# Optimization experiments

Hardware: AMD Instinct MI355X
Metric: run time of the kernel (lower is better)

The kernel has to match this reference:

```python
import jax, jax.numpy as jnp
import numpy as np

B, T, D, FF, H, K = 8, 1024, 512, 2048, 8, 15
HD = D // H  # key_dim = d_model // num_heads


def _ln(x, g, b):
    # keras LayerNormalization default epsilon = 1e-3
    m = jnp.mean(x, axis=-1, keepdims=True)
    v = jnp.var(x, axis=-1, keepdims=True)
    return (x - m) * jax.lax.rsqrt(v + 1e-3) * g + b


def setup_inputs() -> dict:
    key = jax.random.key(0)
    ks = iter(jax.random.split(key, 64))

    def rn(shape, s=0.02):
        return jax.random.normal(next(ks), shape, jnp.float32) * s

    p = {}
    p['x'] = jax.random.normal(next(ks), (B, T, D), jnp.float32)
    # ff_pre: LN -> Dense(FF, relu) -> Dense(D)
    p['g1'] = jnp.ones((D,), jnp.float32); p['b1'] = jnp.zeros((D,), jnp.float32)
    p['Wff1'] = rn((D, FF)); p['bff1'] = jnp.zeros((FF,), jnp.float32)
    p['Wff2'] = rn((FF, D)); p['bff2'] = jnp.zeros((D,), jnp.float32)
    # attention norm + MHA projections (keras EinsumDense shapes)
    p['ga'] = jnp.ones((D,), jnp.float32); p['ba'] = jnp.zeros((D,), jnp.float32)
    p['Wq'] = rn((D, H, HD)); p['bq'] = jnp.zeros((H, HD), jnp.float32)
    p['Wk'] = rn((D, H, HD)); p['bk'] = jnp.zeros((H, HD), jnp.float32)
    p['Wv'] = rn((D, H, HD)); p['bv'] = jnp.zeros((H, HD), jnp.float32)
    p['Wo'] = rn((H, HD, D)); p['bo'] = jnp.zeros((D,), jnp.float32)
    # conv branch: LN -> pointwise conv (2D, gelu) -> depthwise conv(k=15) -> BN -> swish -> pointwise conv (D)
    p['gc'] = jnp.ones((D,), jnp.float32); p['bc'] = jnp.zeros((D,), jnp.float32)
    p['Wcp'] = rn((D, 2 * D)); p['bcp'] = jnp.zeros((2 * D,), jnp.float32)
    p['dwk'] = rn((K, 1, 2 * D)); p['dwb'] = jnp.zeros((2 * D,), jnp.float32)
    p['bn_g'] = jnp.ones((2 * D,), jnp.float32); p['bn_b'] = jnp.zeros((2 * D,), jnp.float32)
    p['bn_m'] = jnp.zeros((2 * D,), jnp.float32)
    p['bn_v'] = jnp.ones((2 * D,), jnp.float32)
    p['Wco'] = rn((2 * D, D)); p['bco'] = jnp.zeros((D,), jnp.float32)
    # ff_post
    p['g2'] = jnp.ones((D,), jnp.float32); p['b2'] = jnp.zeros((D,), jnp.float32)
    p['Wf1'] = rn((D, FF)); p['bf1'] = jnp.zeros((FF,), jnp.float32)
    p['Wf2'] = rn((FF, D)); p['bf2'] = jnp.zeros((D,), jnp.float32)
    return p


def reference(x, g1, b1, Wff1, bff1, Wff2, bff2, ga, ba, Wq, bq, Wk, bk, Wv, bv, Wo, bo, gc, bc, Wcp, bcp, dwk, dwb, bn_g, bn_b, bn_m, bn_v, Wco, bco, g2, b2, Wf1, bf1, Wf2, bf2):
    # Macaron FFN (pre), half-step residual applied later
    x_ff = jnp.maximum(_ln(x, g1, b1) @ Wff1 + bff1, 0.0) @ Wff2 + bff2

    # causal multi-head self-attention (cache=None path)
    a = _ln(x, ga, ba)
    q = jnp.einsum('btd,dhk->bthk', a, Wq) + bq
    k = jnp.einsum('btd,dhk->bthk', a, Wk) + bk
    v = jnp.einsum('btd,dhk->bthk', a, Wv) + bv
    scores = jnp.einsum('bqhd,bkhd->bhqk', q, k) / jnp.sqrt(jnp.float32(HD))
    causal = jnp.tril(jnp.ones((T, T), bool))  # [T,T]
    scores = jnp.where(causal, scores, jnp.float32(-1e9))
    w = jax.nn.softmax(scores, axis=-1)
    ctx = jnp.einsum('bhqk,bkhd->bqhd', w, v)
    attn = jnp.einsum('bqhd,hdo->bqo', ctx, Wo) + bo

    x = x + 0.5 * x_ff + attn

    # convolution module: pointwise(gelu) -> causal left-pad -> depthwise -> BN(inference) -> swish -> pointwise
    c = jax.nn.gelu(_ln(x, gc, bc) @ Wcp + bcp, approximate=False)
    c = jnp.pad(c, ((0, 0), (K - 1, 0), (0, 0)))  # causal pad
    c = jax.lax.conv_general_dilated(
        c, dwk, window_strides=(1,), padding='VALID',
        dimension_numbers=('NWC', 'WIO', 'NWC'), feature_group_count=2 * D) + dwb
    c = (c - bn_m) * jax.lax.rsqrt(bn_v + 1e-3) * bn_g + bn_b
    c = c * jax.nn.sigmoid(c)  # swish
    c = c @ Wco + bco
    x = x + c

    # post FFN (full residual)
    x = x + (jnp.maximum(_ln(x, g2, b2) @ Wf1 + bf1, 0.0) @ Wf2 + bf2)
    return x
```

## Files before the change

kernel.cpp:

```cpp
#include <hip/hip_runtime.h>
#include <hip/hip_bf16.h>
#include <math.h>

#define BB 8
#define TT 1024
#define DD 512
#define FFD 2048
#define HH 8
#define HDD 64
#define KW 15
#define MR (BB*TT)
#define QKVN 1536

typedef __attribute__((ext_vector_type(8))) short short8;
typedef __attribute__((ext_vector_type(4))) short short4v;
typedef __attribute__((ext_vector_type(4))) float f32x4;
typedef __hip_bfloat16 bf16;

__device__ __forceinline__ float bf2f(unsigned u16) {
    return __uint_as_float(u16 << 16);
}

__device__ __forceinline__ void async_copy16(const void* g, void* l) {
    __builtin_amdgcn_global_load_lds(
        (const __attribute__((address_space(1))) void*)g,
        (__attribute__((address_space(3))) void*)l, 16, 0, 0);
}

__device__ __forceinline__ float gelu_exact(float v) {
    return 0.5f * v * (1.0f + erff(v * 0.70710678118654752f));
}

struct PrepPack {
    const float* src[10];
    bf16*        dst[10];
    int          K[10];
    int          lgNT[10];
    float        scale[10];
    int          off[10];
    const float* bq; const float* bk; const float* bv;
    float*       bdst;
    const float* x;
    const float* g1; const float* b1; const float* ga; const float* ba;
    bf16* o1; bf16* o2;
};

__global__ __launch_bounds__(256) void prep_kernel(PrepPack P) {
    __shared__ alignas(16) bf16 T[64][72];
    const int bid = blockIdx.x;
    if (bid == 1536) {
        #pragma unroll
        for (int it = 0; it < 6; ++it) {
            int i = it * 256 + threadIdx.x;
            float v = i < 512 ? P.bq[i] * 0.125f
                              : (i < 1024 ? P.bk[i - 512] : P.bv[i - 1024]);
            P.bdst[i] = v;
        }
        return;
    }
    if (bid > 1536) {
        int wave = ((bid - 1537) * 256 + (int)threadIdx.x) >> 6;
        int lane = threadIdx.x & 63;
        const float* row = P.x + (size_t)wave * DD;
        float4 v0 = ((const float4*)row)[lane];
        float4 v1 = ((const float4*)row)[64 + lane];
        float s  = v0.x + v0.y + v0.z + v0.w + v1.x + v1.y + v1.z + v1.w;
        float ss = v0.x*v0.x + v0.y*v0.y + v0.z*v0.z + v0.w*v0.w
                 + v1.x*v1.x + v1.y*v1.y + v1.z*v1.z + v1.w*v1.w;
        #pragma unroll
        for (int off = 32; off >= 1; off >>= 1) {
            s  += __shfl_xor(s,  off, 64);
            ss += __shfl_xor(ss, off, 64);
        }
        float mean = s * (1.0f / DD);
        float var  = ss * (1.0f / DD) - mean * mean;
        float r    = rsqrtf(var + 1e-3f);
        float n0x = (v0.x - mean) * r, n0y = (v0.y - mean) * r,
              n0z = (v0.z - mean) * r, n0w = (v0.w - mean) * r;
        float n1x = (v1.x - mean) * r, n1y = (v1.y - mean) * r,
              n1z = (v1.z - mean) * r, n1w = (v1.w - mean) * r;
        {
            float4 g0 = ((const float4*)P.g1)[lane];
            float4 gg = ((const float4*)P.g1)[64 + lane];
            float4 b0 = ((const float4*)P.b1)[lane];
            float4 bb = ((const float4*)P.b1)[64 + lane];
            alignas(8) bf16 o0[4], o1[4];
            o0[0] = __float2bfloat16(n0x * g0.x + b0.x);
            o0[1] = __float2bfloat16(n0y * g0.y + b0.y);
            o0[2] = __float2bfloat16(n0z * g0.z + b0.z);
            o0[3] = __float2bfloat16(n0w * g0.w + b0.w);
            o1[0] = __float2bfloat16(n1x * gg.x + bb.x);
            o1[1] = __float2bfloat16(n1y * gg.y + bb.y);
            o1[2] = __float2bfloat16(n1z * gg.z + bb.z);
            o1[3] = __float2bfloat16(n1w * gg.w + bb.w);
            bf16* orow = P.o1 + (size_t)wave * DD;
            *(short4v*)(orow + lane * 4)       = *(const short4v*)o0;
            *(short4v*)(orow + 256 + lane * 4) = *(const short4v*)o1;
        }
        {
            float4 g0 = ((const float4*)P.ga)[lane];
            float4 gg = ((const float4*)P.ga)[64 + lane];
            float4 b0 = ((const float4*)P.ba)[lane];
            float4 bb = ((const float4*)P.ba)[64 + lane];
            alignas(8) bf16 o0[4], o1[4];
            o0[0] = __float2bfloat16(n0x * g0.x + b0.x);
            o0[1] = __float2bfloat16(n0y * g0.y + b0.y);
            o0[2] = __float2bfloat16(n0z * g0.z + b0.z);
            o0[3] = __float2bfloat16(n0w * g0.w + b0.w);
            o1[0] = __float2bfloat16(n1x * gg.x + bb.x);
            o1[1] = __float2bfloat16(n1y * gg.y + bb.y);
            o1[2] = __float2bfloat16(n1z * gg.z + bb.z);
            o1[3] = __float2bfloat16(n1w * gg.w + bb.w);
            bf16* orow = P.o2 + (size_t)wave * DD;
            *(short4v*)(orow + lane * 4)       = *(const short4v*)o0;
            *(short4v*)(orow + 256 + lane * 4) = *(const short4v*)o1;
        }
        return;
    }
    int e = 0;
    #pragma unroll
    for (int i = 1; i < 10; ++i) e = (bid >= P.off[i]) ? i : e;
    const float* W  = P.src[e];
    bf16*        Wt = P.dst[e];
    const int    K  = P.K[e];
    const int    lg = P.lgNT[e];
    const float  scale = P.scale[e];
    const int local = bid - P.off[e];
    const int bx = local & ((1 << lg) - 1);
    const int by = local >> lg;
    const int k0 = by * 64;
    const int n0 = bx * 64;
    const int N  = (1 << lg) * 64;
    const int tid = threadIdx.x;
    #pragma unroll
    for (int it = 0; it < 4; ++it) {
        int lin = it * 256 + tid;
        int kl  = lin >> 4;
        int nq  = (lin & 15) * 4;
        float4 v = *(const float4*)(W + (size_t)(k0 + kl) * N + n0 + nq);
        T[nq + 0][kl] = __float2bfloat16(v.x * scale);
        T[nq + 1][kl] = __float2bfloat16(v.y * scale);
        T[nq + 2][kl] = __float2bfloat16(v.z * scale);
        T[nq + 3][kl] = __float2bfloat16(v.w * scale);
    }
    __syncthreads();
    #pragma unroll
    for (int it = 0; it < 4; ++it) {
        int lin = it * 256 + tid;
        int nl  = lin >> 4;
        int kq  = (lin & 15) * 4;
        *(short4v*)(Wt + (size_t)(n0 + nl) * K + k0 + kq) = *(const short4v*)&T[nl][kq];
    }
}

__global__ __launch_bounds__(256) void ln_kernel(const float* __restrict__ x,
                                                 const float* __restrict__ g,
                                                 const float* __restrict__ b,
                                                 bf16* __restrict__ out) {
    int wave = (blockIdx.x * blockDim.x + threadIdx.x) >> 6;
    int lane = threadIdx.x & 63;
    if (wave >= MR) return;
    const float* row = x + (size_t)wave * DD;
    float4 v0 = ((const float4*)row)[lane];
    float4 v1 = ((const float4*)row)[64 + lane];
    float s  = v0.x + v0.y + v0.z + v0.w + v1.x + v1.y + v1.z + v1.w;
    float ss = v0.x*v0.x + v0.y*v0.y + v0.z*v0.z + v0.w*v0.w
             + v1.x*v1.x + v1.y*v1.y + v1.z*v1.z + v1.w*v1.w;
    #pragma unroll
    for (int off = 32; off >= 1; off >>= 1) {
        s  += __shfl_xor(s,  off, 64);
        ss += __shfl_xor(ss, off, 64);
    }
    float mean = s * (1.0f / DD);
    float var  = ss * (1.0f / DD) - mean * mean;
    float r    = rsqrtf(var + 1e-3f);
    float4 g0 = ((const float4*)g)[lane];
    float4 g1 = ((const float4*)g)[64 + lane];
    float4 b0 = ((const float4*)b)[lane];
    float4 b1 = ((const float4*)b)[64 + lane];
    alignas(8) bf16 o0[4], o1[4];
    o0[0] = __float2bfloat16((v0.x - mean) * r * g0.x + b0.x);
    o0[1] = __float2bfloat16((v0.y - mean) * r * g0.y + b0.y);
    o0[2] = __float2bfloat16((v0.z - mean) * r * g0.z + b0.z);
    o0[3] = __float2bfloat16((v0.w - mean) * r * g0.w + b0.w);
    o1[0] = __float2bfloat16((v1.x - mean) * r * g1.x + b1.x);
    o1[1] = __float2bfloat16((v1.y - mean) * r * g1.y + b1.y);
    o1[2] = __float2bfloat16((v1.z - mean) * r * g1.z + b1.z);
    o1[3] = __float2bfloat16((v1.w - mean) * r * g1.w + b1.w);
    bf16* orow = out + (size_t)wave * DD;
    *(short4v*)(orow + lane * 4)       = *(const short4v*)o0;
    *(short4v*)(orow + 256 + lane * 4) = *(const short4v*)o1;
}

template<int BN, int OP, int RESMODE, int OUTMODE>
__global__ __launch_bounds__(256) void bgemm_kernel(
    const bf16* __restrict__ A,
    const bf16* __restrict__ Bt,
    const float* __restrict__ bias,
    const float* __restrict__ res1,
    const bf16* __restrict__ res2,
    float s2, float oscale,
    void* __restrict__ Cout,
    int N, int Kd, int nxb)
{
    constexpr int NT = BN / 32;
    constexpr int S  = 4 + BN / 32;
    __shared__ alignas(16) bf16 As[2][128][64];
    __shared__ alignas(16) bf16 Bs[2][BN][64];
    const int tid  = threadIdx.x;
    const int w    = tid >> 6;
    const int lane = tid & 63;
    const int quad = lane >> 4;
    const int l16  = lane & 15;
    const int wm   = w >> 1, wn = w & 1;

    const int flat = blockIdx.x;
    const int c8   = flat & 7;
    const int j    = flat >> 3;
    const int jy   = j / nxb;
    const int m0   = (c8 * 8 + jy) * 128;
    const int n0   = (j - jy * nxb) * BN;

    const int srow = lane >> 3;
    const int scol = ((lane & 7) ^ srow) * 8;

    const bf16* Ap = A  + (size_t)(m0 + w * 32 + srow) * Kd + scol;
    const bf16* Bp = Bt + (size_t)(n0 + w * (BN / 4) + srow) * Kd + scol;

    f32x4 acc[4][NT] = {};
    const int nk = Kd >> 6;

#define BSTAGE(bb, kk) do { \
        _Pragma("unroll") \
        for (int i = 0; i < 4; ++i) \
            async_copy16(Ap + (size_t)(i * 8) * Kd + (kk), &As[bb][w * 32 + i * 8][0]); \
        _Pragma("unroll") \
        for (int i = 0; i < BN / 32; ++i) \
            async_copy16(Bp + (size_t)(i * 8) * Kd + (kk), &Bs[bb][w * (BN / 4) + i * 8][0]); \
    } while (0)

    BSTAGE(0, 0);
    for (int t = 0; t < nk; ++t) {
        const int cur = t & 1;
        if (t + 1 < nk) {
            BSTAGE(cur ^ 1, (t + 1) * 64);
            if constexpr (S == 6) asm volatile("s_waitcnt vmcnt(6)" ::: "memory");
            else                  asm volatile("s_waitcnt vmcnt(8)" ::: "memory");
        } else {
            asm volatile("s_waitcnt vmcnt(0)" ::: "memory");
        }
        __builtin_amdgcn_s_barrier();
        __builtin_amdgcn_sched_barrier(0);
        __builtin_amdgcn_s_setprio(1);
        #pragma unroll
        for (int ks = 0; ks < 2; ++ks) {
            short8 af[4], bfr[NT];
            #pragma unroll
            for (int mt = 0; mt < 4; ++mt) {
                const int row = wm * 64 + mt * 16 + l16;
                const int c   = ((ks * 4 + quad) ^ (row & 7)) * 16;
                af[mt] = *(const short8*)((const char*)&As[cur][row][0] + c);
            }
            #pragma unroll
            for (int nt = 0; nt < NT; ++nt) {
                const int col = wn * (BN / 2) + nt * 16 + l16;
                const int c   = ((ks * 4 + quad) ^ (col & 7)) * 16;
                bfr[nt] = *(const short8*)((const char*)&Bs[cur][col][0] + c);
            }
            #pragma unroll
            for (int mt = 0; mt < 4; ++mt)
                #pragma unroll
                for (int nt = 0; nt < NT; ++nt)
                    acc[mt][nt] = __builtin_amdgcn_mfma_f32_16x16x32_bf16(
                        af[mt], bfr[nt], acc[mt][nt], 0, 0, 0);
        }
        __builtin_amdgcn_s_setprio(0);
        asm volatile("" ::: "memory");
        __builtin_amdgcn_s_barrier();
    }
#undef BSTAGE

    const int crow0 = m0 + wm * 64 + quad * 4;
    const int ccol0 = n0 + wn * (BN / 2) + l16;
    #pragma unroll
    for (int nt = 0; nt < NT; ++nt) {
        const int col = ccol0 + nt * 16;
        const float bv = bias[col];
        #pragma unroll
        for (int mt = 0; mt < 4; ++mt) {
            #pragma unroll
            for (int r = 0; r < 4; ++r) {
                const int row = crow0 + mt * 16 + r;
                const size_t off = (size_t)row * N + col;
                float o = acc[mt][nt][r] + bv;
                if (OP == 1)      o = fmaxf(o, 0.f);
                else if (OP == 2) o = gelu_exact(o);
                if (RESMODE >= 1) o += res1[off];
                if (RESMODE == 2) o += s2 * __bfloat162float(res2[off]);
                if (OUTMODE == 0) ((float*)Cout)[off] = o;
                else              ((bf16*)Cout)[off]  = __float2bfloat16(o * oscale);
            }
        }
    }
}

__global__ __launch_bounds__(512, 2) void gemm256_kernel(
    const bf16* __restrict__ Aff, const bf16* __restrict__ Btff,
    const float* __restrict__ biasff, bf16* __restrict__ outff,
    const bf16* __restrict__ Aqk, const bf16* __restrict__ Btqk,
    const float* __restrict__ biasqk, bf16* __restrict__ qkvb,
    bf16* __restrict__ Vtb, int nffblk)
{
    __shared__ alignas(16) char lds[131072];
    const int tid  = threadIdx.x;
    const int w    = tid >> 6;
    const int lane = tid & 63;
    const int quad = lane >> 4;
    const int l16  = lane & 15;
    const int wm   = w >> 2, wn = w & 3;

    const bool jobq = (int)blockIdx.x >= nffblk;
    const int  flat = jobq ? (int)blockIdx.x - nffblk : (int)blockIdx.x;
    const int  nxb  = jobq ? 6 : 8;
    const bf16* A   = jobq ? Aqk : Aff;
    const bf16* Bt  = jobq ? Btqk : Btff;
    const float* bias = jobq ? biasqk : biasff;

    const int c8 = flat & 7;
    const int j  = flat >> 3;
    const int jy = j / nxb;
    const int m0 = (c8 * 4 + jy) * 256;
    const int n0 = (j - jy * nxb) * 256;

    const bf16* ApS = A  + (size_t)(m0 + w * 32 + (lane >> 2)) * DD + (lane & 3) * 8;
    const bf16* BpS = Bt + (size_t)(n0 + w * 32 + (lane >> 2)) * DD + (lane & 3) * 8;
    char* ldsW = lds + w * 2048;

#define STAGE_A(kc, boff) do { \
        async_copy16(ApS + (kc),            ldsW + (boff));        \
        async_copy16(ApS + 16 * DD + (kc),  ldsW + (boff) + 1024); } while (0)
#define STAGE_B(kc, boff) do { \
        async_copy16(BpS + (kc),            ldsW + (boff));        \
        async_copy16(BpS + 16 * DD + (kc),  ldsW + (boff) + 1024); } while (0)

    const int aoff = (wm * 128 + l16) * 64 + quad * 16;
    const int boff = 32768 + (wn * 64 + l16) * 64 + quad * 16;

    f32x4 acc[8][4] = {};

#define CLUSTER(MH) \
    asm volatile("" ::: "memory"); \
    __builtin_amdgcn_s_barrier(); \
    asm volatile("s_waitcnt lgkmcnt(0)" ::: "memory"); \
    __builtin_amdgcn_sched_barrier(0); \
    __builtin_amdgcn_s_setprio(1); \
    _Pragma("unroll") \
    for (int mt = 0; mt < 4; ++mt) \
        _Pragma("unroll") \
        for (int nt = 0; nt < 4; ++nt) \
            acc[(MH) * 4 + mt][nt] = __builtin_amdgcn_mfma_f32_16x16x32_bf16( \
                af[mt], bf[nt], acc[(MH) * 4 + mt][nt], 0, 0, 0); \
    __builtin_amdgcn_s_setprio(0); \
    asm volatile("" ::: "memory"); \
    __builtin_amdgcn_s_barrier();

    STAGE_A(0,  0);      STAGE_B(0,  32768);
    STAGE_A(32, 16384);  STAGE_B(32, 49152);
    STAGE_A(64, 65536);  STAGE_B(64, 65536 + 32768);
    asm volatile("s_waitcnt vmcnt(4)" ::: "memory");
    __builtin_amdgcn_s_barrier();

    for (int t = 0; t < 8; ++t) {
        const int cb = (t & 1) * 65536;
        const int nb = cb ^ 65536;
        short8 af[4], bf[4];

        #pragma unroll
        for (int nt = 0; nt < 4; ++nt)
            bf[nt] = *(const short8*)(lds + cb + boff + nt * 1024);
        #pragma unroll
        for (int mt = 0; mt < 4; ++mt)
            af[mt] = *(const short8*)(lds + cb + aoff + mt * 1024);
        if (t < 7) STAGE_A((t + 1) * 64 + 32, nb + 16384);
        CLUSTER(0)

        #pragma unroll
        for (int mt = 0; mt < 4; ++mt)
            af[mt] = *(const short8*)(lds + cb + aoff + 4096 + mt * 1024);
        if (t < 7) STAGE_B((t + 1) * 64 + 32, nb + 49152);
        CLUSTER(1)

        #pragma unroll
        for (int nt = 0; nt < 4; ++nt)
            bf[nt] = *(const short8*)(lds + cb + 16384 + boff + nt * 1024);
        #pragma unroll
        for (int mt = 0; mt < 4; ++mt)
            af[mt] = *(const short8*)(lds + cb + 16384 + aoff + mt * 1024);
        if (t < 6) STAGE_A((t + 2) * 64, cb);
        CLUSTER(0)

        #pragma unroll
        for (int mt = 0; mt < 4; ++mt)
            af[mt] = *(const short8*)(lds + cb + 16384 + aoff + 4096 + mt * 1024);
        if (t < 6) STAGE_B((t + 2) * 64, cb + 32768);
        if (t < 6)       { asm volatile("s_waitcnt vmcnt(4)" ::: "memory"); }
        else if (t == 6) { asm volatile("s_waitcnt vmcnt(0)" ::: "memory"); }
        CLUSTER(1)
    }
#undef CLUSTER
#undef STAGE_A
#undef STAGE_B

    const int crow0 = m0 + wm * 128 + quad * 4;
    const int ccol0 = n0 + wn * 64 + l16;
    if (jobq) {
        #pragma unroll
        for (int nt = 0; nt < 4; ++nt) {
            const int col = ccol0 + nt * 16;
            const float bv = bias[col];
            #pragma unroll
            for (int mt = 0; mt < 8; ++mt) {
                alignas(8) bf16 o4[4];
                #pragma unroll
                for (int r = 0; r < 4; ++r)
                    o4[r] = __float2bfloat16(acc[mt][nt][r] + bv);
                const int rowt = crow0 + mt * 16;
                if (col < 1024) {
                    #pragma unroll
                    for (int r = 0; r < 4; ++r)
                        qkvb[(size_t)(rowt + r) * QKVN + col] = o4[r];
                } else {
                    const int dg  = col - 1024;
                    const int bb  = rowt >> 10, t0 = rowt & 1023;
                    const int bh2 = bb * 8 + (dg >> 6), d = dg & 63;
                    *(short4v*)(Vtb + ((size_t)bh2 * 64 + d) * TT + t0) =
                        *(const short4v*)o4;
                }
            }
        }
    } else {
        #pragma unroll
        for (int nt = 0; nt < 4; ++nt) {
            const int col = ccol0 + nt * 16;
            const float bv = bias[col];
            #pragma unroll
            for (int mt = 0; mt < 8; ++mt) {
                #pragma unroll
                for (int r = 0; r < 4; ++r) {
                    const float o = fmaxf(acc[mt][nt][r] + bv, 0.f);
                    outff[(size_t)(crow0 + mt * 16 + r) * FFD + col] =
                        __float2bfloat16(o);
                }
            }
        }
    }
}

__global__ __launch_bounds__(256) void ff2attn_kernel(
    const bf16* __restrict__ QKV, const bf16* __restrict__ Vt,
    bf16* __restrict__ ctx,
    const bf16* __restrict__ bigb, const bf16* __restrict__ Wff2t,
    const float* __restrict__ bff2, bf16* __restrict__ xffb)
{
    __shared__ alignas(16) bf16 smem[24576];
    const int tid  = threadIdx.x;
    const int w    = tid >> 6;
    const int lane = tid & 63;
    const int quad = lane >> 4;
    const int l16  = lane & 15;
    const int half = (int)blockIdx.x >> 1;

    if ((blockIdx.x & 1) == 0) {
        typedef bf16 (*tile_t)[64][64];
        tile_t Ks = (tile_t)smem;
        tile_t Vs = (tile_t)(smem + 2 * 64 * 64);
        const int bh = half & 63;
        const int bi = 7 - (half >> 6);
        const int b = bh >> 3, h = bh & 7;

        const bf16* Qg = QKV + (size_t)(b * TT) * QKVN + h * 64;
        const bf16* Kg = QKV + (size_t)(b * TT) * QKVN + 512 + h * 64;
        const bf16* Vg = Vt  + (size_t)bh * 64 * TT;

        const int qL = bi * 128 + w * 16;
        const int qH = qL + 64;
        short8 qfL0 = *(const short8*)(Qg + (size_t)(qL + l16) * QKVN + quad * 8);
        short8 qfL1 = *(const short8*)(Qg + (size_t)(qL + l16) * QKVN + 32 + quad * 8);
        short8 qfH0 = *(const short8*)(Qg + (size_t)(qH + l16) * QKVN + quad * 8);
        short8 qfH1 = *(const short8*)(Qg + (size_t)(qH + l16) * QKVN + 32 + quad * 8);

        const int sgrow  = lane >> 3;
        const int sgchnk = lane & 7;

        f32x4 caccL[4] = {}, caccH[4] = {};
        float lL = 0.f, lH = 0.f;
        const int prow_base = ((l16 >> 2) << 3) + (l16 & 3);
        const int smax = 2 * bi + 1;

        #pragma unroll
        for (int i = 0; i < 2; ++i) {
            const int rowbase = w * 8 + i * 32;
            const int row = rowbase + sgrow;
            const int fR = (row & 3) | (((row >> 3) & 1) << 2);
            const int sc = sgchnk ^ fR;
            async_copy16(Kg + (size_t)row * QKVN + sc * 8, &Ks[0][rowbase][0]);
            async_copy16(Vg + (size_t)row * TT + sc * 8,   &Vs[0][rowbase][0]);
        }

        int buf = 0;
        for (int s = 0; s <= smax; ++s) {
            __syncthreads();
            if (s < smax) {
                const int kn = (s + 1) * 64;
                #pragma unroll
                for (int i = 0; i < 2; ++i) {
                    const int rowbase = w * 8 + i * 32;
                    const int row = rowbase + sgrow;
                    const int fR = (row & 3) | (((row >> 3) & 1) << 2);
                    const int sc = sgchnk ^ fR;
                    async_copy16(Kg + (size_t)(kn + row) * QKVN + sc * 8,
                                 &Ks[buf ^ 1][rowbase][0]);
                    async_copy16(Vg + (size_t)row * TT + kn + sc * 8,
                                 &Vs[buf ^ 1][rowbase][0]);
                }
            }
            const int k0 = s * 64;
            const bool doL = (s < smax);

            f32x4 sTL[4], sTH[4];
            #pragma unroll
            for (int s4 = 0; s4 < 4; ++s4) {
                const int prow = prow_base + (s4 >> 1) * 32 + (s4 & 1) * 4;
                const int fR = (prow & 3) | (((prow >> 3) & 1) << 2);
                short8 ka = *(const short8*)&Ks[buf][prow][(quad ^ fR) * 8];
                short8 kb = *(const short8*)&Ks[buf][prow][((4 + quad) ^ fR) * 8];
                f32x4 zH = {0.f, 0.f, 0.f, 0.f};
                zH = __builtin_amdgcn_mfma_f32_16x16x32_bf16(ka, qfH0, zH, 0, 0, 0);
                sTH[s4] = __builtin_amdgcn_mfma_f32_16x16x32_bf16(kb, qfH1, zH, 0, 0, 0);
                if (doL) {
                    f32x4 zL = {0.f, 0.f, 0.f, 0.f};
                    zL = __builtin_amdgcn_mfma_f32_16x16x32_bf16(ka, qfL0, zL, 0, 0, 0);
                    sTL[s4] = __builtin_amdgcn_mfma_f32_16x16x32_bf16(kb, qfL1, zL, 0, 0, 0);
                }
            }

            alignas(16) bf16 pbH[16], pbL[16];
            if (s == smax) {
                const int qg = qH + l16;
                #pragma unroll
                for (int s4 = 0; s4 < 4; ++s4)
                    #pragma unroll
                    for (int r = 0; r < 4; ++r) {
                        const int key = k0 + (s4 >> 1) * 32 + quad * 8 + (s4 & 1) * 4 + r;
                        const float p = (key <= qg) ? __expf(sTH[s4][r]) : 0.f;
                        lH += p;
                        pbH[s4 * 4 + r] = __float2bfloat16(p);
                    }
            } else {
                #pragma unroll
                for (int s4 = 0; s4 < 4; ++s4)
                    #pragma unroll
                    for (int r = 0; r < 4; ++r) {
                        const float p = __expf(sTH[s4][r]);
                        lH += p;
                        pbH[s4 * 4 + r] = __float2bfloat16(p);
                    }
            }
            if (doL) {
                if (s == smax - 1) {
                    const int qg = qL + l16;
                    #pragma unroll
                    for (int s4 = 0; s4 < 4; ++s4)
                        #pragma unroll
                        for (int r = 0; r < 4; ++r) {
                            const int key = k0 + (s4 >> 1) * 32 + quad * 8 + (s4 & 1) * 4 + r;
                            const float p = (key <= qg) ? __expf(sTL[s4][r]) : 0.f;
                            lL += p;
                            pbL[s4 * 4 + r] = __float2bfloat16(p);
                        }
                } else {
                    #pragma unroll
                    for (int s4 = 0; s4 < 4; ++s4)
                        #pragma unroll
                        for (int r = 0; r < 4; ++r) {
                            const float p = __expf(sTL[s4][r]);
                            lL += p;
                            pbL[s4 * 4 + r] = __float2bfloat16(p);
                        }
                }
            }
            const short8 pfH0 = *(const short8*)&pbH[0];
            const short8 pfH1 = *(const short8*)&pbH[8];
            const short8 pfL0 = *(const short8*)&pbL[0];
            const short8 pfL1 = *(const short8*)&pbL[8];

            #pragma unroll
            for (int g = 0; g < 4; ++g) {
                const int vrow = g * 16 + l16;
                const int fR = (vrow & 3) | (((vrow >> 3) & 1) << 2);
                short8 va = *(const short8*)&Vs[buf][vrow][(quad ^ fR) * 8];
                short8 vb = *(const short8*)&Vs[buf][vrow][((4 + quad) ^ fR) * 8];
                caccH[g] = __builtin_amdgcn_mfma_f32_16x16x32_bf16(va, pfH0, caccH[g], 0, 0, 0);
                caccH[g] = __builtin_amdgcn_mfma_f32_16x16x32_bf16(vb, pfH1, caccH[g], 0, 0, 0);
                if (doL) {
                    caccL[g] = __builtin_amdgcn_mfma_f32_16x16x32_bf16(va, pfL0, caccL[g], 0, 0, 0);
                    caccL[g] = __builtin_amdgcn_mfma_f32_16x16x32_bf16(vb, pfL1, caccL[g], 0, 0, 0);
                }
            }
            buf ^= 1;
        }

        lL += __shfl_xor(lL, 16, 64);
        lL += __shfl_xor(lL, 32, 64);
        lH += __shfl_xor(lH, 16, 64);
        lH += __shfl_xor(lH, 32, 64);
        const float invL = 1.0f / lL;
        const float invH = 1.0f / lH;

        bf16* CbL = ctx + (size_t)(b * TT + qL + l16) * DD + h * 64;
        bf16* CbH = ctx + (size_t)(b * TT + qH + l16) * DD + h * 64;
        #pragma unroll
        for (int g = 0; g < 4; ++g) {
            alignas(8) bf16 oL[4], oH[4];
            #pragma unroll
            for (int r = 0; r < 4; ++r) {
                oL[r] = __float2bfloat16(caccL[g][r] * invL);
                oH[r] = __float2bfloat16(caccH[g][r] * invH);
            }
            *(short4v*)(CbL + g * 16 + quad * 4) = *(const short4v*)oL;
            *(short4v*)(CbH + g * 16 + quad * 4) = *(const short4v*)oH;
        }
    } else {
        const int wm = w >> 1, wn = w & 1;

        const int flat = half;
        const int c8 = flat & 7;
        const int j  = flat >> 3;
        const int jy = j >> 3;
        const int m0 = (c8 * 8 + jy) * 128;
        const int n0 = (j & 7) * 64;

        const int srow = lane >> 3;
        const int scol = ((lane & 7) ^ srow) * 8;

        const bf16* Ap = bigb  + (size_t)(m0 + w * 32 + srow) * FFD + scol;
        const bf16* Bp = Wff2t + (size_t)(n0 + w * 16 + srow) * FFD + scol;

        f32x4 acc[4][2] = {};

#define FSTAGE(bb, kk) do { \
        _Pragma("unroll") \
        for (int i = 0; i < 4; ++i) \
            async_copy16(Ap + (size_t)(i * 8) * FFD + (kk), \
                         smem + (bb) * 8192 + (w * 32 + i * 8) * 64); \
        _Pragma("unroll") \
        for (int i = 0; i < 2; ++i) \
            async_copy16(Bp + (size_t)(i * 8) * FFD + (kk), \
                         smem + 16384 + (bb) * 4096 + (w * 16 + i * 8) * 64); \
    } while (0)

        FSTAGE(0, 0);
        for (int t = 0; t < 32; ++t) {
            const int cur = t & 1;
            if (t < 31) {
                FSTAGE(cur ^ 1, (t + 1) * 64);
                asm volatile("s_waitcnt vmcnt(6)" ::: "memory");
            } else {
                asm volatile("s_waitcnt vmcnt(0)" ::: "memory");
            }
            __builtin_amdgcn_s_barrier();
            __builtin_amdgcn_sched_barrier(0);
            const bf16* AsB = smem + cur * 8192;
            const bf16* BsB = smem + 16384 + cur * 4096;
            __builtin_amdgcn_s_setprio(1);
            #pragma unroll
            for (int ks = 0; ks < 2; ++ks) {
                short8 af[4], bfr[2];
                #pragma unroll
                for (int mt = 0; mt < 4; ++mt) {
                    const int row = wm * 64 + mt * 16 + l16;
                    const int c   = ((ks * 4 + quad) ^ (row & 7)) * 16;
                    af[mt] = *(const short8*)((const char*)(AsB + row * 64) + c);
                }
                #pragma unroll
                for (int nt = 0; nt < 2; ++nt) {
                    const int col = wn * 32 + nt * 16 + l16;
                    const int c   = ((ks * 4 + quad) ^ (col & 7)) * 16;
                    bfr[nt] = *(const short8*)((const char*)(BsB + col * 64) + c);
                }
                #pragma unroll
                for (int mt = 0; mt < 4; ++mt)
                    #pragma unroll
                    for (int nt = 0; nt < 2; ++nt)
                        acc[mt][nt] = __builtin_amdgcn_mfma_f32_16x16x32_bf16(
                            af[mt], bfr[nt], acc[mt][nt], 0, 0, 0);
            }
            __builtin_amdgcn_s_setprio(0);
            asm volatile("" ::: "memory");
            __builtin_amdgcn_s_barrier();
        }
#undef FSTAGE

        const int crow0 = m0 + wm * 64 + quad * 4;
        const int ccol0 = n0 + wn * 32 + l16;
        #pragma unroll
        for (int nt = 0; nt < 2; ++nt) {
            const int col = ccol0 + nt * 16;
            const float bv = bff2[col];
            #pragma unroll
            for (int mt = 0; mt < 4; ++mt)
                #pragma unroll
                for (int r = 0; r < 4; ++r) {
                    const int row = crow0 + mt * 16 + r;
                    xffb[(size_t)row * DD + col] =
                        __float2bfloat16(acc[mt][nt][r] + bv);
                }
        }
    }
}

__global__ __launch_bounds__(256) void dwconv_kernel(const bf16* __restrict__ c1,
                                                     const float* __restrict__ dwk,
                                                     const float* __restrict__ dwb,
                                                     const float* __restrict__ bn_g,
                                                     const float* __restrict__ bn_b,
                                                     const float* __restrict__ bn_m,
                                                     const float* __restrict__ bn_v,
                                                     bf16* __restrict__ out) {
    const int C2 = 2 * DD;
    const int lin = blockIdx.x * 256 + threadIdx.x;
    const int chp = lin & 511;
    const int ch  = chp << 1;
    const int tch = lin >> 9;
    const int row0 = tch << 4;
    const int t0   = row0 & (TT - 1);

    float w0[KW], w1[KW];
    #pragma unroll
    for (int i = 0; i < KW; ++i) {
        w0[i] = dwk[i * C2 + ch];
        w1[i] = dwk[i * C2 + ch + 1];
    }
    const float a0 = rsqrtf(bn_v[ch] + 1e-3f) * bn_g[ch];
    const float a1 = rsqrtf(bn_v[ch + 1] + 1e-3f) * bn_g[ch + 1];
    const float c0 = (dwb[ch] - bn_m[ch]) * a0 + bn_b[ch];
    const float c1v = (dwb[ch + 1] - bn_m[ch + 1]) * a1 + bn_b[ch + 1];

    float x0[30], x1[30];
    if (t0 >= KW - 1) {
        #pragma unroll
        for (int i = 0; i < 30; ++i) {
            unsigned u = *(const unsigned*)(c1 + (size_t)(row0 - (KW - 1) + i) * C2 + ch);
            x0[i] = bf2f(u & 0xffff);
            x1[i] = bf2f(u >> 16);
        }
    } else {
        #pragma unroll
        for (int i = 0; i < 30; ++i) {
            unsigned u = 0;
            if (t0 - (KW - 1) + i >= 0)
                u = *(const unsigned*)(c1 + (size_t)(row0 - (KW - 1) + i) * C2 + ch);
            x0[i] = bf2f(u & 0xffff);
            x1[i] = bf2f(u >> 16);
        }
    }

    #pragma unroll
    for (int j = 0; j < 16; ++j) {
        float s0 = 0.f, s1 = 0.f;
        #pragma unroll
        for (int i = 0; i < KW; ++i) {
            s0 += x0[j + i] * w0[i];
            s1 += x1[j + i] * w1[i];
        }
        s0 = s0 * a0 + c0;
        s1 = s1 * a1 + c1v;
        s0 = s0 / (1.f + __expf(-s0));
        s1 = s1 / (1.f + __expf(-s1));
        alignas(4) bf16 ob[2] = {__float2bfloat16(s0), __float2bfloat16(s1)};
        *(unsigned*)(out + (size_t)(row0 + j) * C2 + ch) = *(const unsigned*)ob;
    }
}

extern "C" void kernel_launch(void* const* d_in, const int* in_sizes, int n_in,
                              void* d_out, int out_size, void* d_ws, size_t ws_size,
                              hipStream_t stream) {
    const float* x    = (const float*)d_in[0];
    const float* g1   = (const float*)d_in[1];
    const float* b1   = (const float*)d_in[2];
    const float* Wff1 = (const float*)d_in[3];
    const float* bff1 = (const float*)d_in[4];
    const float* Wff2 = (const float*)d_in[5];
    const float* bff2 = (const float*)d_in[6];
    const float* ga   = (const float*)d_in[7];
    const float* ba   = (const float*)d_in[8];
    const float* Wq   = (const float*)d_in[9];
    const float* bq   = (const float*)d_in[10];
    const float* Wk   = (const float*)d_in[11];
    const float* bk   = (const float*)d_in[12];
    const float* Wv   = (const float*)d_in[13];
    const float* bv   = (const float*)d_in[14];
    const float* Wo   = (const float*)d_in[15];
    const float* bo   = (const float*)d_in[16];
    const float* gc   = (const float*)d_in[17];
    const float* bc   = (const float*)d_in[18];
    const float* Wcp  = (const float*)d_in[19];
    const float* bcp  = (const float*)d_in[20];
    const float* dwk  = (const float*)d_in[21];
    const float* dwb  = (const float*)d_in[22];
    const float* bn_g = (const float*)d_in[23];
    const float* bn_b = (const float*)d_in[24];
    const float* bn_m = (const float*)d_in[25];
    const float* bn_v = (const float*)d_in[26];
    const float* Wco  = (const float*)d_in[27];
    const float* bco  = (const float*)d_in[28];
    const float* g2   = (const float*)d_in[29];
    const float* b2   = (const float*)d_in[30];
    const float* Wf1  = (const float*)d_in[31];
    const float* bf1  = (const float*)d_in[32];
    const float* Wf2  = (const float*)d_in[33];
    const float* bf2  = (const float*)d_in[34];

    float* out = (float*)d_out;

    char* p = (char*)d_ws;
    bf16* lnb   = (bf16*)p;  p += (size_t)MR * DD * 2;
    bf16* lnab  = (bf16*)p;  p += (size_t)MR * DD * 2;
    bf16* qkvb  = (bf16*)p;  p += (size_t)MR * QKVN * 2;
    bf16* Vtb   = (bf16*)p;  p += (size_t)MR * DD * 2;
    bf16* ctxb  = (bf16*)p;  p += (size_t)MR * DD * 2;
    bf16* xffb  = (bf16*)p;  p += (size_t)MR * DD * 2;
    bf16* bigb  = (bf16*)p;  p += (size_t)MR * FFD * 2;
    bf16* c2b   = (bf16*)p;  p += (size_t)MR * 1024 * 2;
    bf16* Wff1t = (bf16*)p;  p += (size_t)FFD * DD * 2;
    bf16* Wff2t = (bf16*)p;  p += (size_t)DD * FFD * 2;
    bf16* Wqkvt = (bf16*)p;  p += (size_t)QKVN * DD * 2;
    bf16* Wot   = (bf16*)p;  p += (size_t)DD * DD * 2;
    bf16* Wcpt  = (bf16*)p;  p += (size_t)1024 * DD * 2;
    bf16* Wcot  = (bf16*)p;  p += (size_t)DD * 1024 * 2;
    bf16* Wf1t  = (bf16*)p;  p += (size_t)FFD * DD * 2;
    bf16* Wf2t  = (bf16*)p;  p += (size_t)DD * FFD * 2;
    float* bqkv = (float*)p; p += QKVN * 4;

    dim3 blk(256);

    PrepPack P;
    auto set = [&](int i, const float* s, bf16* d, int K, int N, float sc, int off) {
        P.src[i] = s; P.dst[i] = d; P.K[i] = K; P.scale[i] = sc; P.off[i] = off;
        int nt = N / 64, lg = 0; while ((1 << lg) < nt) ++lg; P.lgNT[i] = lg;
    };
    set(0, Wff1, Wff1t, DD,  FFD, 1.f,    0);
    set(1, Wff2, Wff2t, FFD, DD,  1.f,    256);
    set(2, Wq,   Wqkvt,                DD, DD, 0.125f, 512);
    set(3, Wk,   Wqkvt + (size_t)512 * DD,  DD, DD, 1.f, 576);
    set(4, Wv,   Wqkvt + (size_t)1024 * DD, DD, DD, 1.f, 640);
    set(5, Wo,   Wot,   DD,  DD,  1.f,    704);
    set(6, Wcp,  Wcpt,  DD,  1024, 1.f,   768);
    set(7, Wco,  Wcot,  1024, DD, 1.f,    896);
    set(8, Wf1,  Wf1t,  DD,  FFD, 1.f,    1024);
    set(9, Wf2,  Wf2t,  FFD, DD,  1.f,    1280);
    P.bq = bq; P.bk = bk; P.bv = bv; P.bdst = bqkv;
    P.x = x; P.g1 = g1; P.b1 = b1; P.ga = ga; P.ba = ba;
    P.o1 = lnb; P.o2 = lnab;

    prep_kernel<<<dim3(1537 + MR / 4), blk, 0, stream>>>(P);
    gemm256_kernel<<<dim3(448), dim3(512), 0, stream>>>(
        lnb, Wff1t, bff1, bigb, lnab, Wqkvt, bqkv, qkvb, Vtb, 256);
    ff2attn_kernel<<<dim3(1024), blk, 0, stream>>>(
        qkvb, Vtb, ctxb, bigb, Wff2t, bff2, xffb);
    bgemm_kernel<64, 0, 2, 0><<<dim3(8 * 64), blk, 0, stream>>>(
        ctxb, Wot, bo, x, xffb, 0.5f, 1.f, out, DD, DD, 8);
    ln_kernel<<<dim3(MR / 4), blk, 0, stream>>>(out, gc, bc, lnb);
    bgemm_kernel<128, 2, 0, 1><<<dim3(8 * 64), blk, 0, stream>>>(
        lnb, Wcpt, bcp, nullptr, nullptr, 0.f, 1.f, bigb, 1024, DD, 8);
    dwconv_kernel<<<dim3(MR * 512 / 16 / 256), blk, 0, stream>>>(
        bigb, dwk, dwb, bn_g, bn_b, bn_m, bn_v, c2b);
    bgemm_kernel<64, 0, 1, 0><<<dim3(8 * 64), blk, 0, stream>>>(
        c2b, Wcot, bco, out, nullptr, 0.f, 1.f, out, DD, 1024, 8);
    ln_kernel<<<dim3(MR / 4), blk, 0, stream>>>(out, g2, b2, lnb);
    gemm256_kernel<<<dim3(256), dim3(512), 0, stream>>>(
        lnb, Wf1t, bf1, bigb, nullptr, nullptr, nullptr, nullptr, nullptr, 256);
    bgemm_kernel<64, 0, 1, 0><<<dim3(8 * 64), blk, 0, stream>>>(
        bigb, Wf2t, bf2, out, nullptr, 0.f, 1.f, out, DD, FFD, 8);
}
```

Before: 367.0 us.

## Restructure 256x256 GEMM into quadrant tiles with XOR-swizzled 64-wide K LDS staging

Reworks the gemm256 kernel's LDS layout from two 32-wide K halves to a single 64-wide K row of 128 bytes with an XOR swizzle on 16-byte chunks, meant to avoid bank conflicts on the ds_read of MFMA fragments. Each wave now owns a 2x2 grid of quadrant sub-tiles (64x32 per quadrant) instead of a contiguous 128x64 tile. The prefetch of the next K stage is split into four quarter-tile loads interleaved with four compute phases, with adjusted vmcnt waits. The epilogue is rewritten to match the new accumulator mapping. This trades more LDS reads per MFMA and a more intricate wait schedule for conflict-free reads and finer-grained overlap.

```diff
diff --git a/kernel.cpp b/kernel.cpp
--- a/kernel.cpp
+++ b/kernel.cpp
@@ -317,7 +317,7 @@
     const int lane = tid & 63;
     const int quad = lane >> 4;
     const int l16  = lane & 15;
-    const int wm   = w >> 2, wn = w & 3;
+    const int ms   = w >> 2, ns = w & 3;
 
     const bool jobq = (int)blockIdx.x >= nffblk;
     const int  flat = jobq ? (int)blockIdx.x - nffblk : (int)blockIdx.x;
@@ -332,24 +332,45 @@
     const int m0 = (c8 * 4 + jy) * 256;
     const int n0 = (j - jy * nxb) * 256;
 
-    const bf16* ApS = A  + (size_t)(m0 + w * 32 + (lane >> 2)) * DD + (lane & 3) * 8;
-    const bf16* BpS = Bt + (size_t)(n0 + w * 32 + (lane >> 2)) * DD + (lane & 3) * 8;
-    char* ldsW = lds + w * 2048;
-
-#define STAGE_A(kc, boff) do { \
-        async_copy16(ApS + (kc),            ldsW + (boff));        \
-        async_copy16(ApS + 16 * DD + (kc),  ldsW + (boff) + 1024); } while (0)
-#define STAGE_B(kc, boff) do { \
-        async_copy16(BpS + (kc),            ldsW + (boff));        \
-        async_copy16(BpS + 16 * DD + (kc),  ldsW + (boff) + 1024); } while (0)
-
-    const int aoff = (wm * 128 + l16) * 64 + quad * 16;
-    const int boff = 32768 + (wn * 64 + l16) * 64 + quad * 16;
+    const int srow = lane >> 3;
+    const int swz  = ((lane & 7) ^ srow) * 8;
+    const bf16* ApS = A  + (size_t)(m0 + w * 16 + srow) * DD + swz;
+    const bf16* BpS = Bt + (size_t)(n0 + w * 16 + srow) * DD + swz;
+
+#define STG_A(half, kc, nbase) do { \
+        async_copy16(ApS + (size_t)((half) * 128) * DD + (kc), \
+                     lds + (nbase) + (half) * 16384 + (w * 16) * 128); \
+        async_copy16(ApS + (size_t)((half) * 128 + 8) * DD + (kc), \
+                     lds + (nbase) + (half) * 16384 + (w * 16 + 8) * 128); \
+    } while (0)
+#define STG_B(half, kc, nbase) do { \
+        async_copy16(BpS + (size_t)((half) * 128) * DD + (kc), \
+                     lds + (nbase) + 32768 + (half) * 16384 + (w * 16) * 128); \
+        async_copy16(BpS + (size_t)((half) * 128 + 8) * DD + (kc), \
+                     lds + (nbase) + 32768 + (half) * 16384 + (w * 16 + 8) * 128); \
+    } while (0)
+
+    const int cx0  = ((quad)     ^ (l16 & 7)) * 16;
+    const int cx1  = ((4 + quad) ^ (l16 & 7)) * 16;
+    const int arow = (ms * 64 + l16) * 128;
+    const int brow = (ns * 32 + l16) * 128;
 
     f32x4 acc[8][4] = {};
-
-#define CLUSTER(MH) \
-    asm volatile("" ::: "memory"); \
+    short8 a0[4], a1[4], bb0[2], bb1[2];
+
+#define READQ(QM, QN) \
+    _Pragma("unroll") \
+    for (int mt = 0; mt < 4; ++mt) { \
+        a0[mt] = *(const short8*)(lds + cb + (QM) * 16384 + arow + mt * 2048 + cx0); \
+        a1[mt] = *(const short8*)(lds + cb + (QM) * 16384 + arow + mt * 2048 + cx1); \
+    } \
+    _Pragma("unroll") \
+    for (int nt = 0; nt < 2; ++nt) { \
+        bb0[nt] = *(const short8*)(lds + cb + 32768 + (QN) * 16384 + brow + nt * 2048 + cx0); \
+        bb1[nt] = *(const short8*)(lds + cb + 32768 + (QN) * 16384 + brow + nt * 2048 + cx1); \
+    }
+
+#define COMPUTEQ(QM, QN) \
     __builtin_amdgcn_s_barrier(); \
     asm volatile("s_waitcnt lgkmcnt(0)" ::: "memory"); \
     __builtin_amdgcn_sched_barrier(0); \
@@ -357,99 +378,92 @@
     _Pragma("unroll") \
     for (int mt = 0; mt < 4; ++mt) \
         _Pragma("unroll") \
-        for (int nt = 0; nt < 4; ++nt) \
-            acc[(MH) * 4 + mt][nt] = __builtin_amdgcn_mfma_f32_16x16x32_bf16( \
-                af[mt], bf[nt], acc[(MH) * 4 + mt][nt], 0, 0, 0); \
+        for (int nt = 0; nt < 2; ++nt) \
+            acc[(QM) * 4 + mt][(QN) * 2 + nt] = __builtin_amdgcn_mfma_f32_16x16x32_bf16( \
+                a0[mt], bb0[nt], acc[(QM) * 4 + mt][(QN) * 2 + nt], 0, 0, 0); \
+    _Pragma("unroll") \
+    for (int mt = 0; mt < 4; ++mt) \
+        _Pragma("unroll") \
+        for (int nt = 0; nt < 2; ++nt) \
+            acc[(QM) * 4 + mt][(QN) * 2 + nt] = __builtin_amdgcn_mfma_f32_16x16x32_bf16( \
+                a1[mt], bb1[nt], acc[(QM) * 4 + mt][(QN) * 2 + nt], 0, 0, 0); \
     __builtin_amdgcn_s_setprio(0); \
     asm volatile("" ::: "memory"); \
     __builtin_amdgcn_s_barrier();
 
-    STAGE_A(0,  0);      STAGE_B(0,  32768);
-    STAGE_A(32, 16384);  STAGE_B(32, 49152);
-    STAGE_A(64, 65536);  STAGE_B(64, 65536 + 32768);
-    asm volatile("s_waitcnt vmcnt(4)" ::: "memory");
+#define VM4 asm volatile("s_waitcnt vmcnt(4)" ::: "memory")
+#define VM2 asm volatile("s_waitcnt vmcnt(2)" ::: "memory")
+#define VM0 asm volatile("s_waitcnt vmcnt(0)" ::: "memory")
+
+    STG_A(0, 0, 0); STG_B(0, 0, 0); STG_B(1, 0, 0); STG_A(1, 0, 0);
+    VM4;
     __builtin_amdgcn_s_barrier();
 
     for (int t = 0; t < 8; ++t) {
         const int cb = (t & 1) * 65536;
         const int nb = cb ^ 65536;
-        short8 af[4], bf[4];
-
-        #pragma unroll
-        for (int nt = 0; nt < 4; ++nt)
-            bf[nt] = *(const short8*)(lds + cb + boff + nt * 1024);
-        #pragma unroll
-        for (int mt = 0; mt < 4; ++mt)
-            af[mt] = *(const short8*)(lds + cb + aoff + mt * 1024);
-        if (t < 7) STAGE_A((t + 1) * 64 + 32, nb + 16384);
-        CLUSTER(0)
-
-        #pragma unroll
-        for (int mt = 0; mt < 4; ++mt)
-            af[mt] = *(const short8*)(lds + cb + aoff + 4096 + mt * 1024);
-        if (t < 7) STAGE_B((t + 1) * 64 + 32, nb + 49152);
-        CLUSTER(1)
-
-        #pragma unroll
-        for (int nt = 0; nt < 4; ++nt)
-            bf[nt] = *(const short8*)(lds + cb + 16384 + boff + nt * 1024);
-        #pragma unroll
-        for (int mt = 0; mt < 4; ++mt)
-            af[mt] = *(const short8*)(lds + cb + 16384 + aoff + mt * 1024);
-        if (t < 6) STAGE_A((t + 2) * 64, cb);
-        CLUSTER(0)
-
-        #pragma unroll
-        for (int mt = 0; mt < 4; ++mt)
-            af[mt] = *(const short8*)(lds + cb + 16384 + aoff + 4096 + mt * 1024);
-        if (t < 6) STAGE_B((t + 2) * 64, cb + 32768);
-        if (t < 6)       { asm volatile("s_waitcnt vmcnt(4)" ::: "memory"); }
-        else if (t == 6) { asm volatile("s_waitcnt vmcnt(0)" ::: "memory"); }
-        CLUSTER(1)
-    }
-#undef CLUSTER
-#undef STAGE_A
-#undef STAGE_B
-
-    const int crow0 = m0 + wm * 128 + quad * 4;
-    const int ccol0 = n0 + wn * 64 + l16;
-    if (jobq) {
-        #pragma unroll
-        for (int nt = 0; nt < 4; ++nt) {
-            const int col = ccol0 + nt * 16;
+        const int kn = (t + 1) * 64;
+
+        READQ(0, 0)
+        if (t < 7) { STG_A(0, kn, nb); VM4; } else { VM2; }
+        COMPUTEQ(0, 0)
+
+        READQ(0, 1)
+        if (t < 7) { STG_B(0, kn, nb); VM4; } else { VM0; }
+        COMPUTEQ(0, 1)
+
+        READQ(1, 0)
+        if (t < 7) { STG_B(1, kn, nb); VM4; }
+        COMPUTEQ(1, 0)
+
+        READQ(1, 1)
+        if (t < 7) { STG_A(1, kn, nb); VM4; }
+        COMPUTEQ(1, 1)
+    }
+#undef READQ
+#undef COMPUTEQ
+#undef VM4
+#undef VM2
+#undef VM0
+#undef STG_A
+#undef STG_B
+
+    #pragma unroll
+    for (int QN = 0; QN < 2; ++QN) {
+        #pragma unroll
+        for (int nt = 0; nt < 2; ++nt) {
+            const int col = n0 + QN * 128 + ns * 32 + nt * 16 + l16;
             const float bv = bias[col];
             #pragma unroll
-            for (int mt = 0; mt < 8; ++mt) {
-                alignas(8) bf16 o4[4];
+            for (int QM = 0; QM < 2; ++QM) {
                 #pragma unroll
-                for (int r = 0; r < 4; ++r)
-                    o4[r] = __float2bfloat16(acc[mt][nt][r] + bv);
-                const int rowt = crow0 + mt * 16;
-                if (col < 1024) {
-                    #pragma unroll
-                    for (int r = 0; r < 4; ++r)
-                        qkvb[(size_t)(rowt + r) * QKVN + col] = o4[r];
-                } else {
-                    const int dg  = col - 1024;
-                    const int bb  = rowt >> 10, t0 = rowt & 1023;
-                    const int bh2 = bb * 8 + (dg >> 6), d = dg & 63;
-                    *(short4v*)(Vtb + ((size_t)bh2 * 64 + d) * TT + t0) =
-                        *(const short4v*)o4;
-                }
-            }
-        }
-    } else {
-        #pragma unroll
-        for (int nt = 0; nt < 4; ++nt) {
-            const int col = ccol0 + nt * 16;
-            const float bv = bias[col];
-            #pragma unroll
-            for (int mt = 0; mt < 8; ++mt) {
-                #pragma unroll
-                for (int r = 0; r < 4; ++r) {
-                    const float o = fmaxf(acc[mt][nt][r] + bv, 0.f);
-                    outff[(size_t)(crow0 + mt * 16 + r) * FFD + col] =
-                        __float2bfloat16(o);
+                for (int mt = 0; mt < 4; ++mt) {
+                    const f32x4 av = acc[QM * 4 + mt][QN * 2 + nt];
+                    const int rowt = m0 + QM * 128 + ms * 64 + mt * 16 + quad * 4;
+                    if (jobq) {
+                        alignas(8) bf16 o4[4];
+                        #pragma unroll
+                        for (int r = 0; r < 4; ++r)
+                            o4[r] = __float2bfloat16(av[r] + bv);
+                        if (col < 1024) {
+                            #pragma unroll
+                            for (int r = 0; r < 4; ++r)
+                                qkvb[(size_t)(rowt + r) * QKVN + col] = o4[r];
+                        } else {
+                            const int dg  = col - 1024;
+                            const int bb  = rowt >> 10, t0 = rowt & 1023;
+                            const int bh2 = bb * 8 + (dg >> 6), d = dg & 63;
+                            *(short4v*)(Vtb + ((size_t)bh2 * 64 + d) * TT + t0) =
+                                *(const short4v*)o4;
+                        }
+                    } else {
+                        #pragma unroll
+                        for (int r = 0; r < 4; ++r) {
+                            const float o = fmaxf(av[r] + bv, 0.f);
+                            outff[(size_t)(rowt + r) * FFD + col] =
+                                __float2bfloat16(o);
+                        }
+                    }
                 }
             }
         }
```

After: 371.4 us. No clear change (+1.2%).
